# Optimization experiments

Measured on AMD Instinct MI355X. Metric: run time of the kernel, lower is better.

The kernel has to match this reference:

```python
import jax, jax.numpy as jnp
import numpy as np

N_NODES = 50000
N_EDGES = 800000
IN_DIM, HID, OUT = 512, 96, 64


def gcn_conv(x, W, b, src, dst, n_nodes):
    # PyG GCNConv: h = x W; aggregate with sym-normalized adjacency incl. self-loops; add bias.
    h = x @ W  # [N, out]
    ones = jnp.ones_like(dst, dtype=h.dtype)
    deg = jax.ops.segment_sum(ones, dst, num_segments=n_nodes) + 1.0  # +1 for self-loop
    dinv = jax.lax.rsqrt(deg)
    norm = dinv[src] * dinv[dst]  # [E]
    agg = jax.ops.segment_sum(h[src] * norm[:, None], dst, num_segments=n_nodes)
    agg = agg + h * (dinv * dinv)[:, None]  # self-loop messages
    return agg + b


def setup_inputs() -> dict:
    key = jax.random.key(0)
    ks = jax.random.split(key, 12)
    s = 0.05
    x = jax.random.normal(ks[0], (N_NODES, IN_DIM), jnp.float32)
    edge_index = jax.random.randint(ks[1], (2, N_EDGES), 0, N_NODES)
    return {
        "x": x,
        "edge_index": edge_index,
        "W0": jax.random.normal(ks[2], (IN_DIM, HID), jnp.float32) * s,
        "b0": jnp.zeros((HID,), jnp.float32),
        "W1": jax.random.normal(ks[3], (HID, HID), jnp.float32) * s,
        "b1": jnp.zeros((HID,), jnp.float32),
        "W2": jax.random.normal(ks[4], (HID, HID), jnp.float32) * s,
        "b2": jnp.zeros((HID,), jnp.float32),
        "fcW": jax.random.normal(ks[5], (HID, OUT), jnp.float32) * s,
        "fcb": jnp.zeros((OUT,), jnp.float32),
    }


def reference(x, edge_index, W0, b0, W1, b1, W2, b2, fcW, fcb):
    src, dst = edge_index[0], edge_index[1]
    n = x.shape[0]
    # eval mode: dropout is identity; bn=False so no batchnorm
    h = jax.nn.relu(gcn_conv(x, W0, b0, src, dst, n))
    h = jax.nn.relu(gcn_conv(h, W1, b1, src, dst, n))
    h = jax.nn.relu(gcn_conv(h, W2, b2, src, dst, n))
    out = h @ fcW + fcb
    return jnp.squeeze(out)
```

## Files before the change

kernel.cpp:

```cpp
#include <hip/hip_runtime.h>


constexpr int NN   = 50000;
constexpr int NE   = 800000;
constexpr int KIN  = 512;
constexpr int HIDD = 96;
constexpr int ODIM = 64;
constexpr int PAD  = 96;
constexpr int GB   = (NN + 63) / 64;
constexpr int EB   = (NE + 511) / 512;

typedef short bf16x8 __attribute__((ext_vector_type(8)));
typedef short s8v    __attribute__((ext_vector_type(8)));
typedef float f32x4  __attribute__((ext_vector_type(4)));
typedef _Float16 h8  __attribute__((ext_vector_type(8)));
typedef _Float16 h4  __attribute__((ext_vector_type(4)));

__device__ inline short f2bf(float f) {
    union { float f; unsigned u; } v; v.f = f;
    unsigned r = v.u + 0x7FFFu + ((v.u >> 16) & 1u);
    return (short)(r >> 16);
}
__device__ inline short f2bf_trunc(float f) {
    union { float f; unsigned u; } v; v.f = f;
    return (short)(v.u >> 16);
}
__device__ inline float bf2f(short h) {
    union { unsigned u; float f; } v; v.u = ((unsigned)(unsigned short)h) << 16;
    return v.f;
}

__global__ void pack_kernel(const float* __restrict__ W0, const float* __restrict__ W1,
                            const float* __restrict__ W2, const float* __restrict__ FC,
                            short* __restrict__ w0hi, short* __restrict__ w0lo,
                            short* __restrict__ w1hi, short* __restrict__ w1lo,
                            short* __restrict__ w2hi, short* __restrict__ w2lo,
                            short* __restrict__ fchi, short* __restrict__ fclo) {
    const int idx = blockIdx.x * 256 + threadIdx.x;
    const float* W; short *hi, *lo; int M, li;
    if      (idx < 49152) { W = W0; hi = w0hi; lo = w0lo; M = 96; li = idx; }
    else if (idx < 58368) { W = W1; hi = w1hi; lo = w1lo; M = 96; li = idx - 49152; }
    else if (idx < 67584) { W = W2; hi = w2hi; lo = w2lo; M = 96; li = idx - 58368; }
    else if (idx < 73728) { W = FC; hi = fchi; lo = fclo; M = 64; li = idx - 67584; }
    else return;
    const int CT = M >> 4;
    const int j = li & 7;
    const int lane = (li >> 3) & 63;
    const int t = li >> 9;
    const int ct = t % CT;
    const int kc = t / CT;
    const int k = kc * 32 + (lane >> 4) * 8 + j;
    const int n = ct * 16 + (lane & 15);
    const float w = W[k * M + n];
    const short h = f2bf(w);
    hi[li] = h;
    lo[li] = f2bf_trunc(w - bf2f(h));
}

template <int K>
__launch_bounds__(512, 6)
__global__ void gemm_hist(const float* __restrict__ A, const short* __restrict__ Whi,
                          const short* __restrict__ Wlo, float* __restrict__ hs0f, int N,
                          const int* __restrict__ src, const int* __restrict__ dst,
                          int* __restrict__ deg, int* __restrict__ padded) {
    constexpr int CT = 6;
    constexpr int KCH = K / 64;
    constexpr int PH  = KCH / 2;
    __shared__ short sHi[4 * 3072];
    __shared__ short sLo[4 * 3072];

    const int tid = threadIdx.x;
    const int b = blockIdx.x;

    if (b % 3 != 0) {
        const int hb = (2 * b) / 3;
        const int e = hb * 512 + tid;
        if (e < NE) {
            const int d = dst[e];
            const int r = atomicAdd(&deg[d], 1);
            if (r < PAD) padded[d * PAD + r] = src[e];
        }
        return;
    }
    const int gb = b / 3;

    const int lane = tid & 63;
    const int wave = tid >> 6;
    const int rw = wave & 3;
    const int kh = wave >> 2;
    const int q = lane >> 4;
    const int m = lane & 15;
    const int row = gb * 64 + rw * 16 + m;
    const int arow = (row < N) ? row : (N - 1);

    f32x4 acc[CT];
#pragma unroll
    for (int c = 0; c < CT; ++c) acc[c] = f32x4{0.f, 0.f, 0.f, 0.f};

    const float* ap = A + (size_t)arow * K + kh * (K / 2) + q * 8;
    float4 a0 = *(const float4*)(ap);
    float4 a1 = *(const float4*)(ap + 4);

#pragma unroll
    for (int p = 0; p < PH; ++p) {
#pragma unroll
        for (int i = 0; i < 3; ++i) {
            const int ci = i * 512 + tid;
            const int slot = ci / 384;
            const int within = ci - slot * 384;
            const int kcg = (slot >> 1) * KCH + p * 2 + (slot & 1);
            const int so = kcg * 3072 + within * 8;
            const int doff = ci * 8;
            *(float4*)(sHi + doff) = *(const float4*)(Whi + so);
            *(float4*)(sLo + doff) = *(const float4*)(Wlo + so);
        }
        __syncthreads();

#pragma unroll
        for (int kc = 0; kc < 2; ++kc) {
            const float af[8] = {a0.x, a0.y, a0.z, a0.w, a1.x, a1.y, a1.z, a1.w};
            bf16x8 ahi, alo;
#pragma unroll
            for (int j = 0; j < 8; ++j) {
                const short h = f2bf(af[j]);
                ahi[j] = h;
                alo[j] = f2bf_trunc(af[j] - bf2f(h));
            }
            if (p * 2 + kc + 1 < KCH) {
                ap += 32;
                a0 = *(const float4*)(ap);
                a1 = *(const float4*)(ap + 4);
            }
            const int slot = kh * 2 + kc;
            const short* hbase = sHi + slot * 3072 + lane * 8;
            const short* lbase = sLo + slot * 3072 + lane * 8;
#pragma unroll
            for (int c = 0; c < CT; ++c) {
                const bf16x8 wh = *(const bf16x8*)(hbase + c * 512);
                const bf16x8 wl = *(const bf16x8*)(lbase + c * 512);
                acc[c] = __builtin_amdgcn_mfma_f32_16x16x32_bf16(ahi, wh, acc[c], 0, 0, 0);
                acc[c] = __builtin_amdgcn_mfma_f32_16x16x32_bf16(alo, wh, acc[c], 0, 0, 0);
                acc[c] = __builtin_amdgcn_mfma_f32_16x16x32_bf16(ahi, wl, acc[c], 0, 0, 0);
            }
        }
        __syncthreads();
    }

    float* sAcc = (float*)sHi;
    if (kh == 1) {
#pragma unroll
        for (int c = 0; c < CT; ++c)
            *(f32x4*)(sAcc + ((rw * 64 + lane) * CT + c) * 4) = acc[c];
    }
    __syncthreads();
    if (kh == 0) {
#pragma unroll
        for (int c = 0; c < CT; ++c) {
            const f32x4 o = *(const f32x4*)(sAcc + ((rw * 64 + lane) * CT + c) * 4);
            acc[c][0] += o[0]; acc[c][1] += o[1]; acc[c][2] += o[2]; acc[c][3] += o[3];
        }
        const int rbase = gb * 64 + rw * 16 + q * 4;
#pragma unroll
        for (int r = 0; r < 4; ++r) {
            const int orow = rbase + r;
            if (orow < N) {
#pragma unroll
                for (int c = 0; c < CT; ++c)
                    hs0f[(size_t)orow * 96 + c * 16 + m] = acc[c][r];
            }
        }
    }
}

__global__ void dinv_scale(const float* __restrict__ hs0f, const int* __restrict__ deg,
                           float* __restrict__ dinv, _Float16* __restrict__ hsA) {
    const int idx = blockIdx.x * 256 + threadIdx.x;
    if (idx >= NN * 24) return;
    const int row = idx / 24;
    const int c4 = idx - row * 24;
    const float di = 1.0f / sqrtf((float)deg[row] + 1.0f);
    if (c4 == 0) dinv[row] = di;
    const float4 v = *(const float4*)(hs0f + (size_t)row * 96 + c4 * 4);
    h4 o;
    o[0] = (_Float16)(v.x * di);
    o[1] = (_Float16)(v.y * di);
    o[2] = (_Float16)(v.z * di);
    o[3] = (_Float16)(v.w * di);
    *(h4*)(hsA + (size_t)row * 96 + c4 * 4) = o;
}

constexpr int APAD = 104;
template <int M, bool FC>
__launch_bounds__(768, 6)
__global__ void fused_gg(const int* __restrict__ deg, const float* __restrict__ dinv,
                         const int* __restrict__ padded, const _Float16* __restrict__ hs,
                         const float* __restrict__ gb,
                         const short* __restrict__ Whi, const short* __restrict__ Wlo,
                         const float* __restrict__ bias2,
                         _Float16* __restrict__ Ch, float* __restrict__ Cf, int N) {
    constexpr int CT = M / 16;
    __shared__ short sAhi[64 * APAD];
    __shared__ short sAlo[64 * APAD];

    const int tid = threadIdx.x;
    const int nb = blockIdx.x * 64;
    const int nl = tid / 12;
    const int fl = tid - nl * 12;
    const int node = nb + nl;

    s8v hi8, lo8;
    if (node < N) {
        const _Float16* __restrict__ hp = hs + fl * 8;
        float acc0[8], acc1[8];
        {
            const h8 sv = *(const h8*)(hp + (size_t)node * 96);
#pragma unroll
            for (int e = 0; e < 8; ++e) { acc0[e] = (float)sv[e]; acc1[e] = 0.f; }
        }
        const int dg = deg[node];
        int j = node * PAD;
        const int jend = j + (dg < PAD ? dg : PAD);
        for (; j + 8 <= jend; j += 8) {
            const int s0 = padded[j],     s1 = padded[j + 1];
            const int s2 = padded[j + 2], s3 = padded[j + 3];
            const int s4 = padded[j + 4], s5 = padded[j + 5];
            const int s6 = padded[j + 6], s7 = padded[j + 7];
            const h8 v0 = *(const h8*)(hp + (size_t)s0 * 96);
            const h8 v1 = *(const h8*)(hp + (size_t)s1 * 96);
            const h8 v2 = *(const h8*)(hp + (size_t)s2 * 96);
            const h8 v3 = *(const h8*)(hp + (size_t)s3 * 96);
            const h8 v4 = *(const h8*)(hp + (size_t)s4 * 96);
            const h8 v5 = *(const h8*)(hp + (size_t)s5 * 96);
            const h8 v6 = *(const h8*)(hp + (size_t)s6 * 96);
            const h8 v7 = *(const h8*)(hp + (size_t)s7 * 96);
#pragma unroll
            for (int e = 0; e < 8; ++e) {
                acc0[e] += ((float)v0[e] + (float)v4[e]) + ((float)v2[e] + (float)v6[e]);
                acc1[e] += ((float)v1[e] + (float)v5[e]) + ((float)v3[e] + (float)v7[e]);
            }
        }
        if (j + 4 <= jend) {
            const int s0 = padded[j], s1 = padded[j + 1];
            const int s2 = padded[j + 2], s3 = padded[j + 3];
            const h8 v0 = *(const h8*)(hp + (size_t)s0 * 96);
            const h8 v1 = *(const h8*)(hp + (size_t)s1 * 96);
            const h8 v2 = *(const h8*)(hp + (size_t)s2 * 96);
            const h8 v3 = *(const h8*)(hp + (size_t)s3 * 96);
#pragma unroll
            for (int e = 0; e < 8; ++e) {
                acc0[e] += (float)v0[e] + (float)v2[e];
                acc1[e] += (float)v1[e] + (float)v3[e];
            }
            j += 4;
        }
        if (j + 2 <= jend) {
            const int s0 = padded[j], s1 = padded[j + 1];
            const h8 v0 = *(const h8*)(hp + (size_t)s0 * 96);
            const h8 v1 = *(const h8*)(hp + (size_t)s1 * 96);
#pragma unroll
            for (int e = 0; e < 8; ++e) {
                acc0[e] += (float)v0[e];
                acc1[e] += (float)v1[e];
            }
            j += 2;
        }
        if (j < jend) {
            const h8 v0 = *(const h8*)(hp + (size_t)padded[j] * 96);
#pragma unroll
            for (int e = 0; e < 8; ++e) acc0[e] += (float)v0[e];
        }
        const float di = dinv[node];
#pragma unroll
        for (int e = 0; e < 8; ++e) {
            const float o = fmaxf(fmaf(di, acc0[e] + acc1[e], gb[fl * 8 + e]), 0.0f);
            const short h = f2bf(o);
            hi8[e] = h;
            lo8[e] = f2bf_trunc(o - bf2f(h));
        }
    } else {
#pragma unroll
        for (int e = 0; e < 8; ++e) { hi8[e] = 0; lo8[e] = 0; }
    }
    *(s8v*)(sAhi + nl * APAD + fl * 8) = hi8;
    *(s8v*)(sAlo + nl * APAD + fl * 8) = lo8;
    __syncthreads();

    const int lane = tid & 63;
    const int wave = tid >> 6;
    const int rw = wave & 3;
    const int c0 = (wave >> 2) * 2;
    const int q = lane >> 4;
    const int m = lane & 15;

    if (c0 < CT) {
        bf16x8 Ah[3], Al[3];
#pragma unroll
        for (int kc = 0; kc < 3; ++kc) {
            const int off = (rw * 16 + m) * APAD + kc * 32 + q * 8;
            Ah[kc] = *(const bf16x8*)(sAhi + off);
            Al[kc] = *(const bf16x8*)(sAlo + off);
        }

        f32x4 gacc[2];
        gacc[0] = f32x4{0.f, 0.f, 0.f, 0.f};
        gacc[1] = f32x4{0.f, 0.f, 0.f, 0.f};

#pragma unroll
        for (int kc = 0; kc < 3; ++kc) {
#pragma unroll
            for (int c = 0; c < 2; ++c) {
                const int fo = ((kc * CT + c0 + c) * 64 + lane) * 8;
                const bf16x8 wh = *(const bf16x8*)(Whi + fo);
                const bf16x8 wl = *(const bf16x8*)(Wlo + fo);
                gacc[c] = __builtin_amdgcn_mfma_f32_16x16x32_bf16(Ah[kc], wh, gacc[c], 0, 0, 0);
                gacc[c] = __builtin_amdgcn_mfma_f32_16x16x32_bf16(Al[kc], wh, gacc[c], 0, 0, 0);
                gacc[c] = __builtin_amdgcn_mfma_f32_16x16x32_bf16(Ah[kc], wl, gacc[c], 0, 0, 0);
            }
        }

        const int rbase = nb + rw * 16 + q * 4;
#pragma unroll
        for (int r = 0; r < 4; ++r) {
            const int orow = rbase + r;
            if (orow < N) {
                if (FC) {
#pragma unroll
                    for (int c = 0; c < 2; ++c)
                        Cf[(size_t)orow * M + (c0 + c) * 16 + m] = gacc[c][r] + bias2[(c0 + c) * 16 + m];
                } else {
                    const float s = dinv[orow];
#pragma unroll
                    for (int c = 0; c < 2; ++c)
                        Ch[(size_t)orow * M + (c0 + c) * 16 + m] = (_Float16)(gacc[c][r] * s);
                }
            }
        }
    }
}

extern "C" void kernel_launch(void* const* d_in, const int* in_sizes, int n_in,
                              void* d_out, int out_size, void* d_ws, size_t ws_size,
                              hipStream_t stream) {
    const float* x   = (const float*)d_in[0];
    const int*   ei  = (const int*)d_in[1];
    const float* W0  = (const float*)d_in[2];
    const float* b0  = (const float*)d_in[3];
    const float* W1  = (const float*)d_in[4];
    const float* b1  = (const float*)d_in[5];
    const float* W2  = (const float*)d_in[6];
    const float* b2  = (const float*)d_in[7];
    const float* fcW = (const float*)d_in[8];
    const float* fcb = (const float*)d_in[9];
    float* out = (float*)d_out;

    const int* src = ei;
    const int* dst = ei + NE;

    float* ws = (float*)d_ws;
    float* dinv     = ws;
    int*   deg      = (int*)(ws + 50176);
    int*   padded   = (int*)(ws + 100352);
    short* w0hi = (short*)(ws + 4900352);
    short* w0lo = (short*)(ws + 4924928);
    short* w1hi = (short*)(ws + 4949504);
    short* w1lo = (short*)(ws + 4954112);
    short* w2hi = (short*)(ws + 4958720);
    short* w2lo = (short*)(ws + 4963328);
    short* fchi = (short*)(ws + 4967936);
    short* fclo = (short*)(ws + 4971008);
    float* hs0f = ws + 4974080;
    _Float16* hsA = (_Float16*)(ws + 9774080);
    _Float16* hsB = (_Float16*)(ws + 12174080);

    dim3 b256(256);
    const int gPack = (73728 + 255) / 256;
    const int gGH   = GB + EB;
    const int gDS   = (NN * 24 + 255) / 256;
    const int gFus  = GB;

    hipMemsetAsync(deg, 0, NN * sizeof(int), stream);
    pack_kernel<<<gPack, b256, 0, stream>>>(W0, W1, W2, fcW, w0hi, w0lo, w1hi, w1lo,
                                            w2hi, w2lo, fchi, fclo);

    gemm_hist<KIN><<<gGH, dim3(512), 0, stream>>>(x, w0hi, w0lo, hs0f, NN,
                                                  src, dst, deg, padded);

    dinv_scale<<<gDS, b256, 0, stream>>>(hs0f, deg, dinv, hsA);

    fused_gg<HIDD, false><<<gFus, dim3(768), 0, stream>>>(
        deg, dinv, padded, hsA, b0, w1hi, w1lo, nullptr, hsB, nullptr, NN);

    fused_gg<HIDD, false><<<gFus, dim3(768), 0, stream>>>(
        deg, dinv, padded, hsB, b1, w2hi, w2lo, nullptr, hsA, nullptr, NN);

    fused_gg<ODIM, true><<<gFus, dim3(768), 0, stream>>>(
        deg, dinv, padded, hsA, b2, fchi, fclo, fcb, nullptr, out, NN);
}
```

Before: 317.9 us.

## Stage neighbor index lists in LDS and fold degree memset into pack kernel

Each fused gather-GEMM block now copies its 64×96 padded neighbor-index rows into shared memory with coalesced int4 loads before gathering, replacing per-thread scattered global index reads that were repeated by all 12 feature lanes of a node. The self feature and degree loads are issued before the barrier so they can overlap the copy. Separately, the hipMemsetAsync of the degree array is merged into the weight-pack kernel as extra blocks, saving one launch. The change adds 24 KB of LDS per block, which may lower occupancy, and always copies the full padded rows even for low-degree nodes; the last block's copy also reads past NN rows into the padded buffer.

```diff
diff --git a/kernel.cpp b/kernel.cpp
--- a/kernel.cpp
+++ b/kernel.cpp
@@ -7,6 +7,7 @@
 constexpr int HIDD = 96;
 constexpr int ODIM = 64;
 constexpr int PAD  = 96;
+constexpr int NBLK = (NN + 255) / 256;
 constexpr int GB   = (NN + 63) / 64;
 constexpr int EB   = (NE + 511) / 512;
 
@@ -30,13 +31,19 @@
     return v.f;
 }
 
-__global__ void pack_kernel(const float* __restrict__ W0, const float* __restrict__ W1,
-                            const float* __restrict__ W2, const float* __restrict__ FC,
-                            short* __restrict__ w0hi, short* __restrict__ w0lo,
-                            short* __restrict__ w1hi, short* __restrict__ w1lo,
-                            short* __restrict__ w2hi, short* __restrict__ w2lo,
-                            short* __restrict__ fchi, short* __restrict__ fclo) {
-    const int idx = blockIdx.x * 256 + threadIdx.x;
+__global__ void zero_pack(int* __restrict__ deg,
+                          const float* __restrict__ W0, const float* __restrict__ W1,
+                          const float* __restrict__ W2, const float* __restrict__ FC,
+                          short* __restrict__ w0hi, short* __restrict__ w0lo,
+                          short* __restrict__ w1hi, short* __restrict__ w1lo,
+                          short* __restrict__ w2hi, short* __restrict__ w2lo,
+                          short* __restrict__ fchi, short* __restrict__ fclo) {
+    if (blockIdx.x < NBLK) {
+        const int i = blockIdx.x * 256 + threadIdx.x;
+        if (i < NN) deg[i] = 0;
+        return;
+    }
+    const int idx = (blockIdx.x - NBLK) * 256 + threadIdx.x;
     const float* W; short *hi, *lo; int M, li;
     if      (idx < 49152) { W = W0; hi = w0hi; lo = w0lo; M = 96; li = idx; }
     else if (idx < 58368) { W = W1; hi = w1hi; lo = w1lo; M = 96; li = idx - 49152; }
@@ -201,6 +208,7 @@
     constexpr int CT = M / 16;
     __shared__ short sAhi[64 * APAD];
     __shared__ short sAlo[64 * APAD];
+    __shared__ int   sIdx[64 * PAD];
 
     const int tid = threadIdx.x;
     const int nb = blockIdx.x * 64;
@@ -208,23 +216,35 @@
     const int fl = tid - nl * 12;
     const int node = nb + nl;
 
+    {
+        const int4* gp = (const int4*)(padded + (size_t)nb * PAD);
+        int4* sp = (int4*)sIdx;
+        sp[tid] = gp[tid];
+        sp[tid + 768] = gp[tid + 768];
+    }
+
+    int dg = 0;
+    h8 sv;
+    const _Float16* __restrict__ hp = hs + fl * 8;
+    if (node < N) {
+        dg = deg[node];
+        sv = *(const h8*)(hp + (size_t)node * 96);
+    }
+    __syncthreads();
+
     s8v hi8, lo8;
     if (node < N) {
-        const _Float16* __restrict__ hp = hs + fl * 8;
         float acc0[8], acc1[8];
-        {
-            const h8 sv = *(const h8*)(hp + (size_t)node * 96);
-#pragma unroll
-            for (int e = 0; e < 8; ++e) { acc0[e] = (float)sv[e]; acc1[e] = 0.f; }
-        }
-        const int dg = deg[node];
-        int j = node * PAD;
-        const int jend = j + (dg < PAD ? dg : PAD);
-        for (; j + 8 <= jend; j += 8) {
-            const int s0 = padded[j],     s1 = padded[j + 1];
-            const int s2 = padded[j + 2], s3 = padded[j + 3];
-            const int s4 = padded[j + 4], s5 = padded[j + 5];
-            const int s6 = padded[j + 6], s7 = padded[j + 7];
+#pragma unroll
+        for (int e = 0; e < 8; ++e) { acc0[e] = (float)sv[e]; acc1[e] = 0.f; }
+        const int dgc = dg < PAD ? dg : PAD;
+        const int base = nl * PAD;
+        int k = 0;
+        for (; k + 8 <= dgc; k += 8) {
+            const int s0 = sIdx[base + k],     s1 = sIdx[base + k + 1];
+            const int s2 = sIdx[base + k + 2], s3 = sIdx[base + k + 3];
+            const int s4 = sIdx[base + k + 4], s5 = sIdx[base + k + 5];
+            const int s6 = sIdx[base + k + 6], s7 = sIdx[base + k + 7];
             const h8 v0 = *(const h8*)(hp + (size_t)s0 * 96);
             const h8 v1 = *(const h8*)(hp + (size_t)s1 * 96);
             const h8 v2 = *(const h8*)(hp + (size_t)s2 * 96);
@@ -239,9 +259,9 @@
                 acc1[e] += ((float)v1[e] + (float)v5[e]) + ((float)v3[e] + (float)v7[e]);
             }
         }
-        if (j + 4 <= jend) {
-            const int s0 = padded[j], s1 = padded[j + 1];
-            const int s2 = padded[j + 2], s3 = padded[j + 3];
+        if (k + 4 <= dgc) {
+            const int s0 = sIdx[base + k],     s1 = sIdx[base + k + 1];
+            const int s2 = sIdx[base + k + 2], s3 = sIdx[base + k + 3];
             const h8 v0 = *(const h8*)(hp + (size_t)s0 * 96);
             const h8 v1 = *(const h8*)(hp + (size_t)s1 * 96);
             const h8 v2 = *(const h8*)(hp + (size_t)s2 * 96);
@@ -251,10 +271,10 @@
                 acc0[e] += (float)v0[e] + (float)v2[e];
                 acc1[e] += (float)v1[e] + (float)v3[e];
             }
-            j += 4;
-        }
-        if (j + 2 <= jend) {
-            const int s0 = padded[j], s1 = padded[j + 1];
+            k += 4;
+        }
+        if (k + 2 <= dgc) {
+            const int s0 = sIdx[base + k], s1 = sIdx[base + k + 1];
             const h8 v0 = *(const h8*)(hp + (size_t)s0 * 96);
             const h8 v1 = *(const h8*)(hp + (size_t)s1 * 96);
 #pragma unroll
@@ -262,10 +282,10 @@
                 acc0[e] += (float)v0[e];
                 acc1[e] += (float)v1[e];
             }
-            j += 2;
-        }
-        if (j < jend) {
-            const h8 v0 = *(const h8*)(hp + (size_t)padded[j] * 96);
+            k += 2;
+        }
+        if (k < dgc) {
+            const h8 v0 = *(const h8*)(hp + (size_t)sIdx[base + k] * 96);
 #pragma unroll
             for (int e = 0; e < 8; ++e) acc0[e] += (float)v0[e];
         }
@@ -373,14 +393,13 @@
     _Float16* hsB = (_Float16*)(ws + 12174080);
 
     dim3 b256(256);
-    const int gPack = (73728 + 255) / 256;
-    const int gGH   = GB + EB;
-    const int gDS   = (NN * 24 + 255) / 256;
-    const int gFus  = GB;
-
-    hipMemsetAsync(deg, 0, NN * sizeof(int), stream);
-    pack_kernel<<<gPack, b256, 0, stream>>>(W0, W1, W2, fcW, w0hi, w0lo, w1hi, w1lo,
-                                            w2hi, w2lo, fchi, fclo);
+    const int gZP = NBLK + (73728 + 255) / 256;
+    const int gGH = GB + EB;
+    const int gDS = (NN * 24 + 255) / 256;
+    const int gFus = GB;
+
+    zero_pack<<<gZP, b256, 0, stream>>>(deg, W0, W1, W2, fcW, w0hi, w0lo,
+                                        w1hi, w1lo, w2hi, w2lo, fchi, fclo);
 
     gemm_hist<KIN><<<gGH, dim3(512), 0, stream>>>(x, w0hi, w0lo, hs0f, NN,
                                                   src, dst, deg, padded);
```

New measurement: 314.1 us. No clear change (-1.2%).
